# Kernel tuning notes

Hardware: AMD Instinct MI355X
Metric: run time of the kernel (lower is better)

Reference implementation:

```python
import jax, jax.numpy as jnp
import numpy as np

N_NODES = 50000
N_EDGES = 1600000
NODE_DIM = 64
EDGE_DIM = 64
HID = 64
EPS = 1e-5


def _linear(x, W, b):
    return x @ W + b


def _layernorm(x, g, b):
    m = jnp.mean(x, axis=-1, keepdims=True)
    v = jnp.mean((x - m) ** 2, axis=-1, keepdims=True)
    return (x - m) * jax.lax.rsqrt(v + EPS) * g + b


def _mlp(x, p, pre):
    # Linear-ReLU, Linear-ReLU, Linear-LayerNorm
    h = jax.nn.relu(_linear(x, p[pre + 'W1'], p[pre + 'b1']))
    h = jax.nn.relu(_linear(h, p[pre + 'W2'], p[pre + 'b2']))
    h = _linear(h, p[pre + 'W3'], p[pre + 'b3'])
    return _layernorm(h, p[pre + 'g'], p[pre + 'beta'])


def setup_inputs() -> dict:
    key = jax.random.key(0)
    ks = jax.random.split(key, 16)
    inp = {
        'node_feat': jax.random.normal(ks[0], (N_NODES, NODE_DIM), jnp.float32),
        'edge_feat': jax.random.normal(ks[1], (N_EDGES, EDGE_DIM), jnp.float32),
        'edge_idx': jax.random.randint(ks[2], (N_EDGES, 2), 0, N_NODES, jnp.int32),
        'node_size': N_NODES,
    }
    s = 0.05
    e_in = EDGE_DIM + 2 * NODE_DIM
    n_in = NODE_DIM + EDGE_DIM
    inp['eW1'] = jax.random.normal(ks[3], (e_in, HID), jnp.float32) * s
    inp['eb1'] = jnp.zeros((HID,), jnp.float32)
    inp['eW2'] = jax.random.normal(ks[4], (HID, HID), jnp.float32) * s
    inp['eb2'] = jnp.zeros((HID,), jnp.float32)
    inp['eW3'] = jax.random.normal(ks[5], (HID, HID), jnp.float32) * s
    inp['eb3'] = jnp.zeros((HID,), jnp.float32)
    inp['eg'] = jnp.ones((HID,), jnp.float32)
    inp['ebeta'] = jnp.zeros((HID,), jnp.float32)
    inp['nW1'] = jax.random.normal(ks[6], (n_in, HID), jnp.float32) * s
    inp['nb1'] = jnp.zeros((HID,), jnp.float32)
    inp['nW2'] = jax.random.normal(ks[7], (HID, HID), jnp.float32) * s
    inp['nb2'] = jnp.zeros((HID,), jnp.float32)
    inp['nW3'] = jax.random.normal(ks[8], (HID, HID), jnp.float32) * s
    inp['nb3'] = jnp.zeros((HID,), jnp.float32)
    inp['ng'] = jnp.ones((HID,), jnp.float32)
    inp['nbeta'] = jnp.zeros((HID,), jnp.float32)
    return inp


def reference(node_feat, edge_feat, edge_idx, node_size,
              eW1, eb1, eW2, eb2, eW3, eb3, eg, ebeta,
              nW1, nb1, nW2, nb2, nW3, nb3, ng, nbeta):
    p = dict(eW1=eW1, eb1=eb1, eW2=eW2, eb2=eb2, eW3=eW3, eb3=eb3, eg=eg, ebeta=ebeta,
             nW1=nW1, nb1=nb1, nW2=nW2, nb2=nb2, nW3=nW3, nb3=nb3, ng=ng, nbeta=nbeta)
    center = edge_idx[:, 0]
    source = edge_idx[:, 1]
    # [E, edge_dim + 2*node_dim]
    stacked = jnp.concatenate([edge_feat, node_feat[center], node_feat[source]], axis=1)
    proc_edge_feat = _mlp(stacked, p, 'e')  # [E, 64]
    # scatter-add aggregate to nodes
    nodal_edge_feat = jax.ops.segment_sum(proc_edge_feat, center, num_segments=node_size)
    stacked_node = jnp.concatenate([node_feat, nodal_edge_feat], axis=1)  # [N, node_dim+64]
    proc_node_feat = _mlp(stacked_node, p, 'n')  # [N, 64]
    return proc_edge_feat, proc_node_feat
```

## Files before the change

### kernel.cpp

```cpp
#include <hip/hip_runtime.h>

typedef unsigned short u16;
typedef unsigned int u32;
typedef __attribute__((ext_vector_type(8))) __bf16 bf16x8;
typedef __attribute__((ext_vector_type(4))) float f32x4;
typedef __attribute__((ext_vector_type(2))) u32 u32x2;
typedef __attribute__((ext_vector_type(4))) u32 u32x4;

__device__ __forceinline__ u16 f2bf(float f) {
    u32 u = __float_as_uint(f);
    u = (u + 0x7FFFu + ((u >> 16) & 1u)) >> 16;
    return (u16)u;
}

__device__ __forceinline__ bf16x8 load8f_bf(const float* p) {
    f32x4 f0 = *(const f32x4*)p;
    f32x4 f1 = *(const f32x4*)(p + 4);
    bf16x8 r;
    r[0] = (__bf16)f0[0]; r[1] = (__bf16)f0[1]; r[2] = (__bf16)f0[2]; r[3] = (__bf16)f0[3];
    r[4] = (__bf16)f1[0]; r[5] = (__bf16)f1[1]; r[6] = (__bf16)f1[2]; r[7] = (__bf16)f1[3];
    return r;
}
__device__ __forceinline__ bf16x8 cvt2bf(f32x4 lo, f32x4 hi) {
    bf16x8 r;
    r[0] = (__bf16)lo[0]; r[1] = (__bf16)lo[1]; r[2] = (__bf16)lo[2]; r[3] = (__bf16)lo[3];
    r[4] = (__bf16)hi[0]; r[5] = (__bf16)hi[1]; r[6] = (__bf16)hi[2]; r[7] = (__bf16)hi[3];
    return r;
}
__device__ __forceinline__ u32 pk2(float x, float y) {
    __bf16 bx = (__bf16)x, by = (__bf16)y;
    return (u32)__builtin_bit_cast(u16, bx) | ((u32)__builtin_bit_cast(u16, by) << 16);
}

#define PK_EW1 0
#define PK_EW2 12288
#define PK_EW3 16384
#define PK_NW1 20480
#define PK_NW2 28672
#define PK_NW3 32768
#define PK_TOTAL 36864

__global__ void pack_weights_kernel(const float* __restrict__ eW1, const float* __restrict__ eW2,
                                    const float* __restrict__ eW3, const float* __restrict__ nW1,
                                    const float* __restrict__ nW2, const float* __restrict__ nW3,
                                    u16* __restrict__ P) {
    int idx = blockIdx.x * blockDim.x + threadIdx.x;
    if (idx >= PK_TOTAL) return;
    const float* W; int base;
    if (idx < PK_EW2)      { W = eW1; base = PK_EW1; }
    else if (idx < PK_EW3) { W = eW2; base = PK_EW2; }
    else if (idx < PK_NW1) { W = eW3; base = PK_EW3; }
    else if (idx < PK_NW2) { W = nW1; base = PK_NW1; }
    else if (idx < PK_NW3) { W = nW2; base = PK_NW2; }
    else                   { W = nW3; base = PK_NW3; }
    int r = idx - base;
    int j = r & 7, lane = (r >> 3) & 63, m = (r >> 9) & 3, s = r >> 11;
    int k = s * 32 + (lane >> 4) * 8 + j;
    int col = 16 * m + (lane & 15);
    P[idx] = f2bf(W[k * 64 + col]);
}

__global__ void degree_kernel(const int* __restrict__ edge_idx, int* __restrict__ deg, int E) {
    int e = blockIdx.x * blockDim.x + threadIdx.x;
    if (e < E) atomicAdd(&deg[edge_idx[2 * e]], 1);
}

__global__ void scan_blocks_kernel(const int* __restrict__ deg, int* __restrict__ off,
                                   int* __restrict__ partials, int N) {
    __shared__ int sh[256];
    const int t = threadIdx.x;
    const int g = blockIdx.x * 256 + t;
    int v = (g < N) ? deg[g] : 0;
    sh[t] = v;
    __syncthreads();
#pragma unroll
    for (int d = 1; d < 256; d <<= 1) {
        int add = (t >= d) ? sh[t - d] : 0;
        __syncthreads();
        sh[t] += add;
        __syncthreads();
    }
    if (g < N) off[g] = sh[t] - v;
    if (t == 255) partials[blockIdx.x] = sh[255];
}

__global__ void scan_partials_kernel(int* __restrict__ partials, int nparts) {
    __shared__ int sh[256];
    const int t = threadIdx.x;
    int v = (t < nparts) ? partials[t] : 0;
    sh[t] = v;
    __syncthreads();
#pragma unroll
    for (int d = 1; d < 256; d <<= 1) {
        int add = (t >= d) ? sh[t - d] : 0;
        __syncthreads();
        sh[t] += add;
        __syncthreads();
    }
    if (t < nparts) partials[t] = sh[t] - v;
}

__global__ void finalize_offsets_kernel(int* __restrict__ off, int* __restrict__ pos,
                                        const int* __restrict__ partials, int N, int E) {
    int g = blockIdx.x * blockDim.x + threadIdx.x;
    if (g < N) {
        int o = off[g] + partials[g >> 8];
        off[g] = o;
        pos[g] = o;
    }
    if (g == 0) off[N] = E;
}

__global__ void fill_csr_kernel(const int* __restrict__ edge_idx, int* __restrict__ pos,
                                int* __restrict__ csr, int E) {
    int e = blockIdx.x * blockDim.x + threadIdx.x;
    if (e < E) {
        int slot = atomicAdd(&pos[edge_idx[2 * e]], 1);
        csr[slot] = e;
    }
}

#define ET 4
__global__ __launch_bounds__(256) void edge_mlp_kernel(
    const float* __restrict__ node_feat, const float* __restrict__ edge_feat,
    const int* __restrict__ edge_idx, const u16* __restrict__ Pw,
    const float* __restrict__ b1g, const float* __restrict__ b2g, const float* __restrict__ b3g,
    const float* __restrict__ gg, const float* __restrict__ betag,
    float* __restrict__ out_edge, int E)
{
    __shared__ float params[5][64];
    __shared__ u16 htile[4][ET][1024];
    const int tid = threadIdx.x;
    if (tid < 64) {
        params[0][tid] = b1g[tid];
        params[1][tid] = b2g[tid];
        params[2][tid] = b3g[tid];
        params[3][tid] = gg[tid];
        params[4][tid] = betag[tid];
    }
    __syncthreads();
    const int wid = tid >> 6, lane = tid & 63;
    const int er = lane & 15, a = lane >> 4;
    const int ebase = (blockIdx.x * 4 + wid) * (16 * ET);
    if (ebase >= E) return;
    const int swz = (er & 7) << 4;

    int eidx[ET], cn[ET], sn[ET];
#pragma unroll
    for (int t = 0; t < ET; ++t) {
        int e = ebase + t * 16 + er;
        if (e > E - 1) e = E - 1;
        eidx[t] = e;
        int2 ii = *(const int2*)(edge_idx + 2 * e);
        cn[t] = ii.x; sn[t] = ii.y;
    }

    f32x4 acc[ET][4];
#pragma unroll
    for (int t = 0; t < ET; ++t)
#pragma unroll
        for (int m = 0; m < 4; ++m) acc[t][m] = 0.0f;

#pragma unroll
    for (int s = 0; s < 6; ++s) {
        bf16x8 af[4];
#pragma unroll
        for (int m = 0; m < 4; ++m)
            af[m] = *(const bf16x8*)(Pw + PK_EW1 + ((s * 4 + m) * 64 + lane) * 8);
        bf16x8 bf[ET];
#pragma unroll
        for (int t = 0; t < ET; ++t) {
            const float* src;
            if (s < 2)      src = edge_feat + (size_t)eidx[t] * 64 + s * 32 + a * 8;
            else if (s < 4) src = node_feat + (size_t)cn[t] * 64 + (s - 2) * 32 + a * 8;
            else            src = node_feat + (size_t)sn[t] * 64 + (s - 4) * 32 + a * 8;
            bf[t] = load8f_bf(src);
        }
#pragma unroll
        for (int t = 0; t < ET; ++t)
#pragma unroll
            for (int m = 0; m < 4; ++m)
                acc[t][m] = __builtin_amdgcn_mfma_f32_16x16x32_bf16(af[m], bf[t], acc[t][m], 0, 0, 0);
    }
#pragma unroll
    for (int t = 0; t < ET; ++t) {
        u16* ht = htile[wid][t];
#pragma unroll
        for (int m = 0; m < 4; ++m) {
            float v0 = fmaxf(acc[t][m][0] + params[0][16 * m + 4 * a + 0], 0.0f);
            float v1 = fmaxf(acc[t][m][1] + params[0][16 * m + 4 * a + 1], 0.0f);
            float v2 = fmaxf(acc[t][m][2] + params[0][16 * m + 4 * a + 2], 0.0f);
            float v3 = fmaxf(acc[t][m][3] + params[0][16 * m + 4 * a + 3], 0.0f);
            u32x2 pv; pv[0] = pk2(v0, v1); pv[1] = pk2(v2, v3);
            int boff = (er * 128 + (16 * m + 4 * a) * 2) ^ swz;
            *(u32x2*)((char*)ht + boff) = pv;
        }
    }

#pragma unroll
    for (int t = 0; t < ET; ++t)
#pragma unroll
        for (int m = 0; m < 4; ++m) acc[t][m] = 0.0f;
#pragma unroll
    for (int s = 0; s < 2; ++s) {
        bf16x8 af[4];
#pragma unroll
        for (int m = 0; m < 4; ++m)
            af[m] = *(const bf16x8*)(Pw + PK_EW2 + ((s * 4 + m) * 64 + lane) * 8);
#pragma unroll
        for (int t = 0; t < ET; ++t) {
            int boff = (er * 128 + s * 64 + a * 16) ^ swz;
            bf16x8 bf = *(const bf16x8*)((char*)htile[wid][t] + boff);
#pragma unroll
            for (int m = 0; m < 4; ++m)
                acc[t][m] = __builtin_amdgcn_mfma_f32_16x16x32_bf16(af[m], bf, acc[t][m], 0, 0, 0);
        }
    }
#pragma unroll
    for (int t = 0; t < ET; ++t) {
        u16* ht = htile[wid][t];
#pragma unroll
        for (int m = 0; m < 4; ++m) {
            float v0 = fmaxf(acc[t][m][0] + params[1][16 * m + 4 * a + 0], 0.0f);
            float v1 = fmaxf(acc[t][m][1] + params[1][16 * m + 4 * a + 1], 0.0f);
            float v2 = fmaxf(acc[t][m][2] + params[1][16 * m + 4 * a + 2], 0.0f);
            float v3 = fmaxf(acc[t][m][3] + params[1][16 * m + 4 * a + 3], 0.0f);
            u32x2 pv; pv[0] = pk2(v0, v1); pv[1] = pk2(v2, v3);
            int boff = (er * 128 + (16 * m + 4 * a) * 2) ^ swz;
            *(u32x2*)((char*)ht + boff) = pv;
        }
    }

#pragma unroll
    for (int t = 0; t < ET; ++t)
#pragma unroll
        for (int m = 0; m < 4; ++m) acc[t][m] = 0.0f;
#pragma unroll
    for (int s = 0; s < 2; ++s) {
        bf16x8 af[4];
#pragma unroll
        for (int m = 0; m < 4; ++m)
            af[m] = *(const bf16x8*)(Pw + PK_EW3 + ((s * 4 + m) * 64 + lane) * 8);
#pragma unroll
        for (int t = 0; t < ET; ++t) {
            int boff = (er * 128 + s * 64 + a * 16) ^ swz;
            bf16x8 bf = *(const bf16x8*)((char*)htile[wid][t] + boff);
#pragma unroll
            for (int m = 0; m < 4; ++m)
                acc[t][m] = __builtin_amdgcn_mfma_f32_16x16x32_bf16(af[m], bf, acc[t][m], 0, 0, 0);
        }
    }
#pragma unroll
    for (int t = 0; t < ET; ++t) {
        float vals[16], sum = 0.0f, ssq = 0.0f;
#pragma unroll
        for (int m = 0; m < 4; ++m)
#pragma unroll
            for (int r = 0; r < 4; ++r) {
                float v = acc[t][m][r] + params[2][16 * m + 4 * a + r];
                vals[4 * m + r] = v; sum += v; ssq += v * v;
            }
        sum += __shfl_xor(sum, 16, 64); sum += __shfl_xor(sum, 32, 64);
        ssq += __shfl_xor(ssq, 16, 64); ssq += __shfl_xor(ssq, 32, 64);
        const float mean = sum * 0.015625f;
        const float var = ssq * 0.015625f - mean * mean;
        const float inv = rsqrtf(var + 1e-5f);
        const int e = ebase + t * 16 + er;
        if (e < E) {
#pragma unroll
            for (int m = 0; m < 4; ++m) {
                f32x4 o;
#pragma unroll
                for (int r = 0; r < 4; ++r) {
                    int f = 16 * m + 4 * a + r;
                    o[r] = (vals[4 * m + r] - mean) * inv * params[3][f] + params[4][f];
                }
                *(f32x4*)(out_edge + (size_t)e * 64 + 16 * m + 4 * a) = o;
            }
        }
    }
}

__global__ __launch_bounds__(256) void node_mlp_kernel(
    const float* __restrict__ node_feat, const float* __restrict__ proc_edge,
    const int* __restrict__ off, const int* __restrict__ csr,
    const u16* __restrict__ Pw,
    const float* __restrict__ b1g, const float* __restrict__ b2g, const float* __restrict__ b3g,
    const float* __restrict__ gg, const float* __restrict__ betag,
    float* __restrict__ out_node, int N)
{
    __shared__ float params[5][64];
    __shared__ u16 htile[4][1024];
    const int tid = threadIdx.x;
    if (tid < 64) {
        params[0][tid] = b1g[tid];
        params[1][tid] = b2g[tid];
        params[2][tid] = b3g[tid];
        params[3][tid] = gg[tid];
        params[4][tid] = betag[tid];
    }
    __syncthreads();
    const int wid = tid >> 6, lane = tid & 63;
    const int er = lane & 15, a = lane >> 4;
    const int nbase = (blockIdx.x * 4 + wid) * 16;
    if (nbase >= N) return;
    const int n = nbase + er;
    u16* ht = htile[wid];
    const int swz = (er & 7) << 4;

    f32x4 g0a = 0.0f, g0b = 0.0f, g1a = 0.0f, g1b = 0.0f;
    {
        const int beg = off[n], end = off[n + 1];
        int j = beg;
        for (; j + 3 < end; j += 4) {
#pragma unroll
            for (int u = 0; u < 4; ++u) {
                const float* row = proc_edge + (size_t)csr[j + u] * 64;
                g0a += *(const f32x4*)(row + a * 8);
                g0b += *(const f32x4*)(row + a * 8 + 4);
                g1a += *(const f32x4*)(row + 32 + a * 8);
                g1b += *(const f32x4*)(row + 32 + a * 8 + 4);
            }
        }
        for (; j < end; ++j) {
            const float* row = proc_edge + (size_t)csr[j] * 64;
            g0a += *(const f32x4*)(row + a * 8);
            g0b += *(const f32x4*)(row + a * 8 + 4);
            g1a += *(const f32x4*)(row + 32 + a * 8);
            g1b += *(const f32x4*)(row + 32 + a * 8 + 4);
        }
    }

    f32x4 acc[4];
#pragma unroll
    for (int m = 0; m < 4; ++m) acc[m] = 0.0f;

#pragma unroll
    for (int s = 0; s < 4; ++s) {
        bf16x8 af[4];
#pragma unroll
        for (int m = 0; m < 4; ++m)
            af[m] = *(const bf16x8*)(Pw + PK_NW1 + ((s * 4 + m) * 64 + lane) * 8);
        bf16x8 bf;
        if (s < 2)       bf = load8f_bf(node_feat + (size_t)n * 64 + s * 32 + a * 8);
        else if (s == 2) bf = cvt2bf(g0a, g0b);
        else             bf = cvt2bf(g1a, g1b);
#pragma unroll
        for (int m = 0; m < 4; ++m)
            acc[m] = __builtin_amdgcn_mfma_f32_16x16x32_bf16(af[m], bf, acc[m], 0, 0, 0);
    }
#pragma unroll
    for (int m = 0; m < 4; ++m) {
        float v0 = fmaxf(acc[m][0] + params[0][16 * m + 4 * a + 0], 0.0f);
        float v1 = fmaxf(acc[m][1] + params[0][16 * m + 4 * a + 1], 0.0f);
        float v2 = fmaxf(acc[m][2] + params[0][16 * m + 4 * a + 2], 0.0f);
        float v3 = fmaxf(acc[m][3] + params[0][16 * m + 4 * a + 3], 0.0f);
        u32x2 pv; pv[0] = pk2(v0, v1); pv[1] = pk2(v2, v3);
        int boff = (er * 128 + (16 * m + 4 * a) * 2) ^ swz;
        *(u32x2*)((char*)ht + boff) = pv;
    }

#pragma unroll
    for (int m = 0; m < 4; ++m) acc[m] = 0.0f;
#pragma unroll
    for (int s = 0; s < 2; ++s) {
        bf16x8 af[4];
#pragma unroll
        for (int m = 0; m < 4; ++m)
            af[m] = *(const bf16x8*)(Pw + PK_NW2 + ((s * 4 + m) * 64 + lane) * 8);
        int boff = (er * 128 + s * 64 + a * 16) ^ swz;
        bf16x8 bf = *(const bf16x8*)((char*)ht + boff);
#pragma unroll
        for (int m = 0; m < 4; ++m)
            acc[m] = __builtin_amdgcn_mfma_f32_16x16x32_bf16(af[m], bf, acc[m], 0, 0, 0);
    }
#pragma unroll
    for (int m = 0; m < 4; ++m) {
        float v0 = fmaxf(acc[m][0] + params[1][16 * m + 4 * a + 0], 0.0f);
        float v1 = fmaxf(acc[m][1] + params[1][16 * m + 4 * a + 1], 0.0f);
        float v2 = fmaxf(acc[m][2] + params[1][16 * m + 4 * a + 2], 0.0f);
        float v3 = fmaxf(acc[m][3] + params[1][16 * m + 4 * a + 3], 0.0f);
        u32x2 pv; pv[0] = pk2(v0, v1); pv[1] = pk2(v2, v3);
        int boff = (er * 128 + (16 * m + 4 * a) * 2) ^ swz;
        *(u32x2*)((char*)ht + boff) = pv;
    }

#pragma unroll
    for (int m = 0; m < 4; ++m) acc[m] = 0.0f;
#pragma unroll
    for (int s = 0; s < 2; ++s) {
        bf16x8 af[4];
#pragma unroll
        for (int m = 0; m < 4; ++m)
            af[m] = *(const bf16x8*)(Pw + PK_NW3 + ((s * 4 + m) * 64 + lane) * 8);
        int boff = (er * 128 + s * 64 + a * 16) ^ swz;
        bf16x8 bf = *(const bf16x8*)((char*)ht + boff);
#pragma unroll
        for (int m = 0; m < 4; ++m)
            acc[m] = __builtin_amdgcn_mfma_f32_16x16x32_bf16(af[m], bf, acc[m], 0, 0, 0);
    }
    float vals[16], sum = 0.0f, ssq = 0.0f;
#pragma unroll
    for (int m = 0; m < 4; ++m)
#pragma unroll
        for (int r = 0; r < 4; ++r) {
            float v = acc[m][r] + params[2][16 * m + 4 * a + r];
            vals[4 * m + r] = v; sum += v; ssq += v * v;
        }
    sum += __shfl_xor(sum, 16, 64); sum += __shfl_xor(sum, 32, 64);
    ssq += __shfl_xor(ssq, 16, 64); ssq += __shfl_xor(ssq, 32, 64);
    const float mean = sum * 0.015625f;
    const float var = ssq * 0.015625f - mean * mean;
    const float inv = rsqrtf(var + 1e-5f);
#pragma unroll
    for (int m = 0; m < 4; ++m) {
        f32x4 o;
#pragma unroll
        for (int r = 0; r < 4; ++r) {
            int f = 16 * m + 4 * a + r;
            o[r] = (vals[4 * m + r] - mean) * inv * params[3][f] + params[4][f];
        }
        *(f32x4*)(out_node + (size_t)n * 64 + 16 * m + 4 * a) = o;
    }
}

extern "C" void kernel_launch(void* const* d_in, const int* in_sizes, int n_in,
                              void* d_out, int out_size, void* d_ws, size_t ws_size,
                              hipStream_t stream) {
    const float* node_feat = (const float*)d_in[0];
    const float* edge_feat = (const float*)d_in[1];
    const int* edge_idx  = (const int*)d_in[2];
    const float* eW1 = (const float*)d_in[4];
    const float* eb1 = (const float*)d_in[5];
    const float* eW2 = (const float*)d_in[6];
    const float* eb2 = (const float*)d_in[7];
    const float* eW3 = (const float*)d_in[8];
    const float* eb3 = (const float*)d_in[9];
    const float* eg  = (const float*)d_in[10];
    const float* ebt = (const float*)d_in[11];
    const float* nW1 = (const float*)d_in[12];
    const float* nb1 = (const float*)d_in[13];
    const float* nW2 = (const float*)d_in[14];
    const float* nb2 = (const float*)d_in[15];
    const float* nW3 = (const float*)d_in[16];
    const float* nb3 = (const float*)d_in[17];
    const float* ng  = (const float*)d_in[18];
    const float* nbt = (const float*)d_in[19];

    const int N = in_sizes[0] / 64;
    const int E = in_sizes[1] / 64;
    const int nparts = (N + 255) / 256;

    char* w = (char*)d_ws;
    int* off      = (int*)w;                    w += (size_t)(N + 1) * 4;
    int* pos      = (int*)w;                    w += (size_t)N * 4;
    int* partials = (int*)w;                    w += 256 * 4;
    int* csr      = (int*)w;                    w += (size_t)E * 4;
    u16* Pw       = (u16*)w;

    float* out_edge = (float*)d_out;
    float* out_node = out_edge + (size_t)E * 64;

    pack_weights_kernel<<<(PK_TOTAL + 255) / 256, 256, 0, stream>>>(eW1, eW2, eW3, nW1, nW2, nW3, Pw);

    const int eblocks = (E + 255) / 256;
    edge_mlp_kernel<<<eblocks, 256, 0, stream>>>(node_feat, edge_feat, edge_idx, Pw,
                                                 eb1, eb2, eb3, eg, ebt, out_edge, E);

    hipMemsetAsync(pos, 0, (size_t)N * 4, stream);
    degree_kernel<<<(E + 255) / 256, 256, 0, stream>>>(edge_idx, pos, E);
    scan_blocks_kernel<<<nparts, 256, 0, stream>>>(pos, off, partials, N);
    scan_partials_kernel<<<1, 256, 0, stream>>>(partials, nparts);
    finalize_offsets_kernel<<<(N + 255) / 256, 256, 0, stream>>>(off, pos, partials, N, E);
    fill_csr_kernel<<<(E + 255) / 256, 256, 0, stream>>>(edge_idx, pos, csr, E);

    const int nblocks = (N + 63) / 64;
    node_mlp_kernel<<<nblocks, 256, 0, stream>>>(node_feat, out_edge, off, csr, Pw,
                                                 nb1, nb2, nb3, ng, nbt, out_node, N);
}
```

Measured before the change: 630.1 us.

## Halve edge tile, process layers 2-3 per tile, shrink LDS buffer

The edge MLP kernel now handles two 16-edge tiles per wave instead of four. Layers 2 and 3 and the LayerNorm run tile by tile using one shared LDS scratch buffer per wave instead of one buffer per tile. This cuts accumulator registers and LDS use, which should allow more waves per CU, at the cost of reloading layer-2/3 weights for each tile and launching more blocks. The node kernel's gather loop is also unrolled from 4 to 8 edges to keep more loads in flight.

Result: slower. 648.1 us (+2.8%).

```diff
diff --git a/kernel.cpp b/kernel.cpp
--- a/kernel.cpp
+++ b/kernel.cpp
@@ -120,7 +120,7 @@
     }
 }
 
-#define ET 4
+#define ET 2
 __global__ __launch_bounds__(256) void edge_mlp_kernel(
     const float* __restrict__ node_feat, const float* __restrict__ edge_feat,
     const int* __restrict__ edge_idx, const u16* __restrict__ Pw,
@@ -129,7 +129,7 @@
     float* __restrict__ out_edge, int E)
 {
     __shared__ float params[5][64];
-    __shared__ u16 htile[4][ET][1024];
+    __shared__ u16 htile[4][1024];
     const int tid = threadIdx.x;
     if (tid < 64) {
         params[0][tid] = b1g[tid];
@@ -143,6 +143,7 @@
     const int er = lane & 15, a = lane >> 4;
     const int ebase = (blockIdx.x * 4 + wid) * (16 * ET);
     if (ebase >= E) return;
+    u16* ht = htile[wid];
     const int swz = (er & 7) << 4;
 
     int eidx[ET], cn[ET], sn[ET];
@@ -182,9 +183,9 @@
             for (int m = 0; m < 4; ++m)
                 acc[t][m] = __builtin_amdgcn_mfma_f32_16x16x32_bf16(af[m], bf[t], acc[t][m], 0, 0, 0);
     }
+
 #pragma unroll
     for (int t = 0; t < ET; ++t) {
-        u16* ht = htile[wid][t];
 #pragma unroll
         for (int m = 0; m < 4; ++m) {
             float v0 = fmaxf(acc[t][m][0] + params[0][16 * m + 4 * a + 0], 0.0f);
@@ -195,69 +196,52 @@
             int boff = (er * 128 + (16 * m + 4 * a) * 2) ^ swz;
             *(u32x2*)((char*)ht + boff) = pv;
         }
-    }
-
-#pragma unroll
-    for (int t = 0; t < ET; ++t)
-#pragma unroll
-        for (int m = 0; m < 4; ++m) acc[t][m] = 0.0f;
-#pragma unroll
-    for (int s = 0; s < 2; ++s) {
-        bf16x8 af[4];
-#pragma unroll
-        for (int m = 0; m < 4; ++m)
-            af[m] = *(const bf16x8*)(Pw + PK_EW2 + ((s * 4 + m) * 64 + lane) * 8);
-#pragma unroll
-        for (int t = 0; t < ET; ++t) {
+        f32x4 a2[4];
+#pragma unroll
+        for (int m = 0; m < 4; ++m) a2[m] = 0.0f;
+#pragma unroll
+        for (int s = 0; s < 2; ++s) {
+            bf16x8 af[4];
+#pragma unroll
+            for (int m = 0; m < 4; ++m)
+                af[m] = *(const bf16x8*)(Pw + PK_EW2 + ((s * 4 + m) * 64 + lane) * 8);
             int boff = (er * 128 + s * 64 + a * 16) ^ swz;
-            bf16x8 bf = *(const bf16x8*)((char*)htile[wid][t] + boff);
+            bf16x8 bf = *(const bf16x8*)((char*)ht + boff);
 #pragma unroll
             for (int m = 0; m < 4; ++m)
-                acc[t][m] = __builtin_amdgcn_mfma_f32_16x16x32_bf16(af[m], bf, acc[t][m], 0, 0, 0);
-        }
-    }
-#pragma unroll
-    for (int t = 0; t < ET; ++t) {
-        u16* ht = htile[wid][t];
+                a2[m] = __builtin_amdgcn_mfma_f32_16x16x32_bf16(af[m], bf, a2[m], 0, 0, 0);
+        }
 #pragma unroll
         for (int m = 0; m < 4; ++m) {
-            float v0 = fmaxf(acc[t][m][0] + params[1][16 * m + 4 * a + 0], 0.0f);
-            float v1 = fmaxf(acc[t][m][1] + params[1][16 * m + 4 * a + 1], 0.0f);
-            float v2 = fmaxf(acc[t][m][2] + params[1][16 * m + 4 * a + 2], 0.0f);
-            float v3 = fmaxf(acc[t][m][3] + params[1][16 * m + 4 * a + 3], 0.0f);
+            float v0 = fmaxf(a2[m][0] + params[1][16 * m + 4 * a + 0], 0.0f);
+            float v1 = fmaxf(a2[m][1] + params[1][16 * m + 4 * a + 1], 0.0f);
+            float v2 = fmaxf(a2[m][2] + params[1][16 * m + 4 * a + 2], 0.0f);
+            float v3 = fmaxf(a2[m][3] + params[1][16 * m + 4 * a + 3], 0.0f);
             u32x2 pv; pv[0] = pk2(v0, v1); pv[1] = pk2(v2, v3);
             int boff = (er * 128 + (16 * m + 4 * a) * 2) ^ swz;
             *(u32x2*)((char*)ht + boff) = pv;
         }
-    }
-
-#pragma unroll
-    for (int t = 0; t < ET; ++t)
-#pragma unroll
-        for (int m = 0; m < 4; ++m) acc[t][m] = 0.0f;
-#pragma unroll
-    for (int s = 0; s < 2; ++s) {
-        bf16x8 af[4];
-#pragma unroll
-        for (int m = 0; m < 4; ++m)
-            af[m] = *(const bf16x8*)(Pw + PK_EW3 + ((s * 4 + m) * 64 + lane) * 8);
-#pragma unroll
-        for (int t = 0; t < ET; ++t) {
+        f32x4 a3[4];
+#pragma unroll
+        for (int m = 0; m < 4; ++m) a3[m] = 0.0f;
+#pragma unroll
+        for (int s = 0; s < 2; ++s) {
+            bf16x8 af[4];
+#pragma unroll
+            for (int m = 0; m < 4; ++m)
+                af[m] = *(const bf16x8*)(Pw + PK_EW3 + ((s * 4 + m) * 64 + lane) * 8);
             int boff = (er * 128 + s * 64 + a * 16) ^ swz;
-            bf16x8 bf = *(const bf16x8*)((char*)htile[wid][t] + boff);
+            bf16x8 bf = *(const bf16x8*)((char*)ht + boff);
 #pragma unroll
             for (int m = 0; m < 4; ++m)
-                acc[t][m] = __builtin_amdgcn_mfma_f32_16x16x32_bf16(af[m], bf, acc[t][m], 0, 0, 0);
-        }
-    }
-#pragma unroll
-    for (int t = 0; t < ET; ++t) {
+                a3[m] = __builtin_amdgcn_mfma_f32_16x16x32_bf16(af[m], bf, a3[m], 0, 0, 0);
+        }
         float vals[16], sum = 0.0f, ssq = 0.0f;
 #pragma unroll
         for (int m = 0; m < 4; ++m)
 #pragma unroll
             for (int r = 0; r < 4; ++r) {
-                float v = acc[t][m][r] + params[2][16 * m + 4 * a + r];
+                float v = a3[m][r] + params[2][16 * m + 4 * a + r];
                 vals[4 * m + r] = v; sum += v; ssq += v * v;
             }
         sum += __shfl_xor(sum, 16, 64); sum += __shfl_xor(sum, 32, 64);
@@ -312,9 +296,9 @@
     {
         const int beg = off[n], end = off[n + 1];
         int j = beg;
-        for (; j + 3 < end; j += 4) {
-#pragma unroll
-            for (int u = 0; u < 4; ++u) {
+        for (; j + 7 < end; j += 8) {
+#pragma unroll
+            for (int u = 0; u < 8; ++u) {
                 const float* row = proc_edge + (size_t)csr[j + u] * 64;
                 g0a += *(const f32x4*)(row + a * 8);
                 g0b += *(const f32x4*)(row + a * 8 + 4);
@@ -463,7 +447,7 @@
 
     pack_weights_kernel<<<(PK_TOTAL + 255) / 256, 256, 0, stream>>>(eW1, eW2, eW3, nW1, nW2, nW3, Pw);
 
-    const int eblocks = (E + 255) / 256;
+    const int eblocks = (E + (64 * ET) - 1) / (64 * ET);
     edge_mlp_kernel<<<eblocks, 256, 0, stream>>>(node_feat, edge_feat, edge_idx, Pw,
                                                  eb1, eb2, eb3, eg, ebt, out_edge, E);
 
```
